# Kernel optimization log

Measured on AMD Instinct MI355X. Metric: run time of the kernel, lower is better.

## Reference

```python
import jax, jax.numpy as jnp
import numpy as np
import math

ATTN_C = 32
HEADS = 8
IN_C = 256
PAIR_C = 128
B, M, N = 1, 128, 256


def _layernorm(x, w, b, eps=1e-5):
    mu = jnp.mean(x, axis=-1, keepdims=True)
    xc = x - mu
    var = jnp.mean(xc * xc, axis=-1, keepdims=True)
    return xc * jax.lax.rsqrt(var + eps) * w + b


def setup_inputs() -> dict:
    key = jax.random.key(0)
    ks = jax.random.split(key, 10)
    s1 = 1.0 / math.sqrt(IN_C)
    s2 = 1.0 / math.sqrt(PAIR_C)
    s3 = 1.0 / math.sqrt(ATTN_C * HEADS)
    return {
        "x1d": jax.random.normal(ks[0], (B, M, N, IN_C), jnp.float32),
        "x2d": jax.random.normal(ks[1], (B, N, N, PAIR_C), jnp.float32),
        "norm_w": jnp.ones((IN_C,), jnp.float32),
        "norm_b": jnp.zeros((IN_C,), jnp.float32),
        "qkv_w": jax.random.normal(ks[2], (3 * ATTN_C * HEADS, IN_C), jnp.float32) * s1,
        "x2d_w": jax.random.normal(ks[3], (HEADS, PAIR_C), jnp.float32) * s2,
        "gate_w": jax.random.normal(ks[4], (ATTN_C * HEADS, IN_C), jnp.float32) * s1,
        "gate_b": jnp.zeros((ATTN_C * HEADS,), jnp.float32),
        "final_w": jax.random.normal(ks[5], (IN_C, ATTN_C * HEADS), jnp.float32) * s3,
        "final_b": jnp.zeros((IN_C,), jnp.float32),
    }


def reference(x1d, x2d, norm_w, norm_b, qkv_w, x2d_w, gate_w, gate_b, final_w, final_b):
    c, h = ATTN_C, HEADS
    x = _layernorm(x1d, norm_w, norm_b)                      # [B,M,N,IN_C]
    qkv = (x @ qkv_w.T).reshape(*x.shape[:-1], c, 3 * h)     # [B,M,N,c,3h]
    q, k, v = qkv[..., :h], qkv[..., h:2 * h], qkv[..., 2 * h:]
    aff = jnp.einsum('bmich,bmjch->bmijh', q, k)             # [B,M,N,N,H]
    gate = jax.nn.sigmoid(x @ gate_w.T + gate_b).reshape(*x.shape[:-1], c, h)
    factor = 1.0 / math.sqrt(c)
    bias = (x2d @ x2d_w.T) * factor                          # [B,N,N,H]
    weights = jax.nn.softmax(aff + bias[:, None], axis=-2)   # softmax over j
    out = jnp.einsum('bmrch,bmirh->bmich', v, weights) * gate
    out = out.reshape(*x.shape[:-1], c * h) @ final_w.T + final_b
    return out
```

## Files before the change

kernel.cpp:

```cpp
#include <hip/hip_runtime.h>
#include <math.h>

typedef short bf16x8 __attribute__((ext_vector_type(8)));
typedef float f32x4  __attribute__((ext_vector_type(4)));

#define NPOS 32768

#define OFF_CHI   0u
#define OFF_AHI   100663296u
#define OFF_ATTN  134217728u
#define OFF_BIAST 150994944u
#define OFF_WHI   153354240u
#define OFF_W2P   154402816u
#define OFF_GBP   154533888u

__device__ __forceinline__ short f2bf(float x) {
    unsigned int u = __float_as_uint(x);
    unsigned int r = (u + 0x7FFFu + ((u >> 16) & 1u)) >> 16;
    return (short)r;
}
__device__ __forceinline__ float bf2f(short s) {
    return __uint_as_float(((unsigned int)(unsigned short)s) << 16);
}
__device__ __forceinline__ void async_copy16(const void* g, void* l) {
    __builtin_amdgcn_global_load_lds(
        (const __attribute__((address_space(1))) unsigned int*)g,
        (__attribute__((address_space(3))) unsigned int*)l, 16, 0, 0);
}

__global__ void k_ln_cast(const float* __restrict__ x,
                          const float* __restrict__ nw, const float* __restrict__ nb,
                          short* __restrict__ Ahi) {
    int wid = (blockIdx.x * blockDim.x + threadIdx.x) >> 6;
    int lane = threadIdx.x & 63;
    const float4 v = ((const float4*)(x + (size_t)wid * 256))[lane];
    float s  = v.x + v.y + v.z + v.w;
    float ss = v.x*v.x + v.y*v.y + v.z*v.z + v.w*v.w;
    #pragma unroll
    for (int o = 32; o; o >>= 1) {
        s  += __shfl_xor(s,  o, 64);
        ss += __shfl_xor(ss, o, 64);
    }
    float mu  = s * (1.0f / 256);
    float var = ss * (1.0f / 256) - mu * mu;
    float rs  = rsqrtf(var + 1e-5f);
    const float4 wv = ((const float4*)nw)[lane];
    const float4 bv = ((const float4*)nb)[lane];
    float y[4] = {(v.x - mu) * rs * wv.x + bv.x, (v.y - mu) * rs * wv.y + bv.y,
                  (v.z - mu) * rs * wv.z + bv.z, (v.w - mu) * rs * wv.w + bv.w};
    short h4[4];
    #pragma unroll
    for (int i = 0; i < 4; ++i) h4[i] = f2bf(y[i]);
    *(short4*)(Ahi + (size_t)wid * 256 + lane * 4) = *(short4*)h4;
}

__global__ void k_castw(const float* __restrict__ qkvw, const float* __restrict__ gatew,
                        const float* __restrict__ gateb, const float* __restrict__ finalw,
                        short* __restrict__ Whi, short* __restrict__ W2p,
                        float* __restrict__ gbp) {
    int r = blockIdx.x, t = threadIdx.x;
    if (r < 1024) {
        int which = r >> 8, h = (r >> 5) & 7, c = r & 31;
        const float* src = (which < 3) ? qkvw + (size_t)(c * 24 + which * 8 + h) * 256
                                       : gatew + (size_t)(c * 8 + h) * 256;
        Whi[(size_t)r * 256 + t] = f2bf(src[t]);
    } else if (r < 1280) {
        int o = r - 1024;
        int h = t >> 5, c = t & 31;
        W2p[(size_t)o * 256 + t] = f2bf(finalw[(size_t)o * 256 + c * 8 + h]);
    } else {
        int h = t >> 5, c = t & 31;
        gbp[t] = gateb[c * 8 + h];
    }
}

__global__ __launch_bounds__(256) void k_bias2(const float* __restrict__ x2d,
                                               const float* __restrict__ x2dw,
                                               float* __restrict__ biasT) {
    __shared__ float xs[64][132];
    __shared__ float ws[8][132];
    const int t = threadIdx.x;
    const int wid0 = blockIdx.x * 64;
    #pragma unroll
    for (int r = 0; r < 8; ++r) {
        int g = r * 256 + t;
        int row = g >> 5, c4 = g & 31;
        float4 v = *(const float4*)(x2d + (size_t)(wid0 + row) * 128 + c4 * 4);
        *(float4*)&xs[row][c4 * 4] = v;
    }
    {
        int h = t >> 5, c4 = t & 31;
        *(float4*)&ws[h][c4 * 4] = *(const float4*)(x2dw + h * 128 + c4 * 4);
    }
    __syncthreads();
    const float f = 0.17677669529663687f;
    const int i = wid0 >> 8;
    #pragma unroll
    for (int kk = 0; kk < 2; ++kk) {
        int o = t + kk * 256;
        int row = o >> 3, h = o & 7;
        float acc = 0.f;
        #pragma unroll
        for (int c4 = 0; c4 < 32; ++c4) {
            float4 xv = *(const float4*)&xs[row][c4 * 4];
            float4 wv = *(const float4*)&ws[h][c4 * 4];
            acc += xv.x * wv.x + xv.y * wv.y + xv.z * wv.z + xv.w * wv.w;
        }
        int j = (wid0 & 255) + row;
        biasT[(((h * 256 + j)) << 8) + i] = acc * f;
    }
}

__global__ __launch_bounds__(256) void k_gemm1m(
    const short* __restrict__ Ahi, const short* __restrict__ Whi,
    const float* __restrict__ gbp, short* __restrict__ Chi) {
    __shared__ short As[128 * 64];
    __shared__ short Bs[128 * 64];
    const int t = threadIdx.x;
    const int wave = t >> 6, lane = t & 63, ln15 = lane & 15, quad = lane >> 4;
    const int posBase = blockIdx.x * 128;
    const int nb = blockIdx.y;
    const int i0w = (wave & 1) * 64, n0w = (wave >> 1) * 64;

    f32x4 acc[4][4];
    #pragma unroll
    for (int a = 0; a < 4; ++a)
        #pragma unroll
        for (int b = 0; b < 4; ++b) acc[a][b] = (f32x4){0.f, 0.f, 0.f, 0.f};

    for (int k0 = 0; k0 < 256; k0 += 64) {
        #pragma unroll
        for (int r = 0; r < 4; ++r) {
            int g = r * 256 + t;
            int row = g >> 3, cs = g & 7;
            int colg = cs ^ (row & 7);
            size_t aoff = (size_t)(posBase + row) * 256 + k0 + colg * 8;
            size_t boff = (size_t)(nb * 128 + row) * 256 + k0 + colg * 8;
            int ldst = (r * 256 + wave * 64) * 8;
            async_copy16(Ahi + aoff, &As[ldst]);
            async_copy16(Whi + boff, &Bs[ldst]);
        }
        __syncthreads();
        #pragma unroll
        for (int kc = 0; kc < 2; ++kc) {
            bf16x8 af[4], bfr[4];
            #pragma unroll
            for (int it = 0; it < 4; ++it) {
                int rowa = i0w + it * 16 + ln15;
                int c8a = (kc * 4 + quad) ^ (rowa & 7);
                af[it] = *(const bf16x8*)&As[rowa * 64 + c8a * 8];
                int rowb = n0w + it * 16 + ln15;
                int c8b = (kc * 4 + quad) ^ (rowb & 7);
                bfr[it] = *(const bf16x8*)&Bs[rowb * 64 + c8b * 8];
            }
            #pragma unroll
            for (int it = 0; it < 4; ++it)
                #pragma unroll
                for (int nt = 0; nt < 4; ++nt)
                    acc[it][nt] = __builtin_amdgcn_mfma_f32_16x16x32_bf16(
                        bfr[nt], af[it], acc[it][nt], 0, 0, 0);
        }
        __syncthreads();
    }
    const bool isgate = (nb >= 6);
    #pragma unroll
    for (int it = 0; it < 4; ++it) {
        size_t pos = posBase + i0w + it * 16 + ln15;
        #pragma unroll
        for (int nt = 0; nt < 4; ++nt) {
            int ncol0 = nb * 128 + n0w + nt * 16 + quad * 4;
            float v[4];
            #pragma unroll
            for (int r = 0; r < 4; ++r) v[r] = acc[it][nt][r];
            if (isgate) {
                const float4 gb = *(const float4*)&gbp[ncol0 - 768];
                v[0] = 1.0f / (1.0f + __expf(-(v[0] + gb.x)));
                v[1] = 1.0f / (1.0f + __expf(-(v[1] + gb.y)));
                v[2] = 1.0f / (1.0f + __expf(-(v[2] + gb.z)));
                v[3] = 1.0f / (1.0f + __expf(-(v[3] + gb.w)));
            }
            unsigned w0 = (unsigned)(unsigned short)f2bf(v[0])
                        | ((unsigned)(unsigned short)f2bf(v[1]) << 16);
            unsigned w1 = (unsigned)(unsigned short)f2bf(v[2])
                        | ((unsigned)(unsigned short)f2bf(v[3]) << 16);
            *(uint2*)&Chi[pos * 1024 + ncol0] = make_uint2(w0, w1);
        }
    }
}

__global__ __launch_bounds__(512) void k_attn3(
    const short* __restrict__ Chi, const float* __restrict__ biasT,
    short* __restrict__ attnB) {
    __shared__ short Khi[256 * 32];
    __shared__ short VT[32 * 264];
    __shared__ short Pl[8][16][40];

    const int mh = blockIdx.x;
    const int m = mh >> 3, h = mh & 7;
    const int t = threadIdx.x;
    const int wave = t >> 6, lane = t & 63, ln15 = lane & 15, quad = lane >> 4;
    const int i0 = wave * 32;

    #pragma unroll
    for (int r = 0; r < 2; ++r) {
        int g = r * 512 + t;
        int j = g >> 2, c16 = g & 3;
        int cs = c16 ^ (j & 3);
        const short* gp = Chi + (size_t)(m * 256 + j) * 1024 + 256 + h * 32 + cs * 8;
        async_copy16(gp, &Khi[(r * 512 + wave * 64) * 8]);
    }
    {
        int j = t & 255, c0 = (t >> 8) * 16;
        const short* vp = Chi + (size_t)(m * 256 + j) * 1024 + 512 + h * 32 + c0;
        bf16x8 v0 = *(const bf16x8*)vp;
        bf16x8 v1 = *(const bf16x8*)(vp + 8);
        #pragma unroll
        for (int c = 0; c < 8; ++c) VT[(c0 + c) * 264 + j] = v0[c];
        #pragma unroll
        for (int c = 0; c < 8; ++c) VT[(c0 + 8 + c) * 264 + j] = v1[c];
    }
    bf16x8 qhi[2];
    #pragma unroll
    for (int it = 0; it < 2; ++it) {
        int i = i0 + it * 16 + ln15;
        qhi[it] = *(const bf16x8*)(Chi + (size_t)(m * 256 + i) * 1024 + h * 32 + quad * 8);
    }
    __syncthreads();

    float lacc[2] = {0.f, 0.f};
    f32x4 Oacc[2][2];
    #pragma unroll
    for (int a = 0; a < 2; ++a) {
        Oacc[a][0] = (f32x4){0.f, 0.f, 0.f, 0.f};
        Oacc[a][1] = (f32x4){0.f, 0.f, 0.f, 0.f};
    }
    const float* bp = biasT + (size_t)h * 65536;

    for (int j0 = 0; j0 < 256; j0 += 32) {
        bf16x8 kfh[2], vf[2];
        #pragma unroll
        for (int jt = 0; jt < 2; ++jt) {
            int j = j0 + jt * 16 + ln15;
            int cs = quad ^ (j & 3);
            kfh[jt] = *(const bf16x8*)&Khi[j * 32 + cs * 8];
        }
        #pragma unroll
        for (int ct = 0; ct < 2; ++ct) {
            int c = ct * 16 + ln15;
            vf[ct] = *(const bf16x8*)&VT[c * 264 + j0 + quad * 8];
        }
        #pragma unroll
        for (int it = 0; it < 2; ++it) {
            int i = i0 + it * 16 + ln15;
            float b0[4], b1[4];
            #pragma unroll
            for (int r = 0; r < 4; ++r) {
                b0[r] = bp[(j0 + quad * 4 + r) * 256 + i];
                b1[r] = bp[(j0 + 16 + quad * 4 + r) * 256 + i];
            }
            f32x4 s0 = (f32x4){0.f, 0.f, 0.f, 0.f};
            f32x4 s1 = (f32x4){0.f, 0.f, 0.f, 0.f};
            s0 = __builtin_amdgcn_mfma_f32_16x16x32_bf16(kfh[0], qhi[it], s0, 0, 0, 0);
            s1 = __builtin_amdgcn_mfma_f32_16x16x32_bf16(kfh[1], qhi[it], s1, 0, 0, 0);
            float p[8], ps = 0.f;
            #pragma unroll
            for (int r = 0; r < 4; ++r) { p[r] = __expf(s0[r] + b0[r]); ps += p[r]; }
            #pragma unroll
            for (int r = 0; r < 4; ++r) { p[4 + r] = __expf(s1[r] + b1[r]); ps += p[4 + r]; }
            lacc[it] += ps;
            unsigned long long pw0 =
                  (unsigned long long)(unsigned short)f2bf(p[0])
                | ((unsigned long long)(unsigned short)f2bf(p[1]) << 16)
                | ((unsigned long long)(unsigned short)f2bf(p[2]) << 32)
                | ((unsigned long long)(unsigned short)f2bf(p[3]) << 48);
            unsigned long long pw1 =
                  (unsigned long long)(unsigned short)f2bf(p[4])
                | ((unsigned long long)(unsigned short)f2bf(p[5]) << 16)
                | ((unsigned long long)(unsigned short)f2bf(p[6]) << 32)
                | ((unsigned long long)(unsigned short)f2bf(p[7]) << 48);
            *(unsigned long long*)&Pl[wave][ln15][quad * 4]      = pw0;
            *(unsigned long long*)&Pl[wave][ln15][16 + quad * 4] = pw1;
            bf16x8 pf = *(const bf16x8*)&Pl[wave][ln15][quad * 8];
            Oacc[it][0] = __builtin_amdgcn_mfma_f32_16x16x32_bf16(pf, vf[0], Oacc[it][0], 0, 0, 0);
            Oacc[it][1] = __builtin_amdgcn_mfma_f32_16x16x32_bf16(pf, vf[1], Oacc[it][1], 0, 0, 0);
        }
    }
    #pragma unroll
    for (int it = 0; it < 2; ++it) {
        float l = lacc[it];
        l += __shfl_xor(l, 16, 64);
        l += __shfl_xor(l, 32, 64);
        float inv = 1.0f / l;
        float invr[4];
        #pragma unroll
        for (int r = 0; r < 4; ++r) invr[r] = __shfl(inv, quad * 4 + r, 16);
        #pragma unroll
        for (int ct = 0; ct < 2; ++ct) {
            int c = ct * 16 + ln15;
            #pragma unroll
            for (int r = 0; r < 4; ++r) {
                int i = i0 + it * 16 + quad * 4 + r;
                float g = bf2f(Chi[(size_t)(m * 256 + i) * 1024 + 768 + h * 32 + c]);
                float val = Oacc[it][ct][r] * invr[r] * g;
                attnB[(size_t)(m * 256 + i) * 256 + h * 32 + c] = f2bf(val);
            }
        }
    }
}

__global__ __launch_bounds__(256) void k_gemm2m(
    const short* __restrict__ A, const short* __restrict__ W2p,
    const float* __restrict__ fb, float* __restrict__ out) {
    __shared__ short As[128 * 64];
    __shared__ short Bs[128 * 64];
    const int t = threadIdx.x;
    const int wave = t >> 6, lane = t & 63, ln15 = lane & 15, quad = lane >> 4;
    const int posBase = blockIdx.x * 128;
    const int nb = blockIdx.y;
    const int i0w = (wave & 1) * 64, n0w = (wave >> 1) * 64;

    f32x4 acc[4][4];
    #pragma unroll
    for (int a = 0; a < 4; ++a)
        #pragma unroll
        for (int b = 0; b < 4; ++b) acc[a][b] = (f32x4){0.f, 0.f, 0.f, 0.f};

    for (int k0 = 0; k0 < 256; k0 += 64) {
        #pragma unroll
        for (int r = 0; r < 4; ++r) {
            int g = r * 256 + t;
            int row = g >> 3, cs = g & 7;
            int colg = cs ^ (row & 7);
            const short* ga = A + (size_t)(posBase + row) * 256 + k0 + colg * 8;
            async_copy16(ga, &As[(r * 256 + wave * 64) * 8]);
            const short* gb = W2p + (size_t)(nb * 128 + row) * 256 + k0 + colg * 8;
            async_copy16(gb, &Bs[(r * 256 + wave * 64) * 8]);
        }
        __syncthreads();
        #pragma unroll
        for (int kc = 0; kc < 2; ++kc) {
            bf16x8 af[4], bfr[4];
            #pragma unroll
            for (int it = 0; it < 4; ++it) {
                int rowa = i0w + it * 16 + ln15;
                int c8a = (kc * 4 + quad) ^ (rowa & 7);
                af[it] = *(const bf16x8*)&As[rowa * 64 + c8a * 8];
                int rowb = n0w + it * 16 + ln15;
                int c8b = (kc * 4 + quad) ^ (rowb & 7);
                bfr[it] = *(const bf16x8*)&Bs[rowb * 64 + c8b * 8];
            }
            #pragma unroll
            for (int it = 0; it < 4; ++it)
                #pragma unroll
                for (int nt = 0; nt < 4; ++nt)
                    acc[it][nt] = __builtin_amdgcn_mfma_f32_16x16x32_bf16(
                        bfr[nt], af[it], acc[it][nt], 0, 0, 0);
        }
        __syncthreads();
    }
    #pragma unroll
    for (int it = 0; it < 4; ++it) {
        size_t pos = posBase + i0w + it * 16 + ln15;
        #pragma unroll
        for (int nt = 0; nt < 4; ++nt) {
            int ncol0 = nb * 128 + n0w + nt * 16 + quad * 4;
            const float4 fbv = *(const float4*)&fb[ncol0];
            float4 o;
            o.x = acc[it][nt][0] + fbv.x;
            o.y = acc[it][nt][1] + fbv.y;
            o.z = acc[it][nt][2] + fbv.z;
            o.w = acc[it][nt][3] + fbv.w;
            *(float4*)&out[pos * 256 + ncol0] = o;
        }
    }
}

extern "C" void kernel_launch(void* const* d_in, const int* in_sizes, int n_in,
                              void* d_out, int out_size, void* d_ws, size_t ws_size,
                              hipStream_t stream) {
    const float* x1d     = (const float*)d_in[0];
    const float* x2d     = (const float*)d_in[1];
    const float* norm_w  = (const float*)d_in[2];
    const float* norm_b  = (const float*)d_in[3];
    const float* qkv_w   = (const float*)d_in[4];
    const float* x2d_w   = (const float*)d_in[5];
    const float* gate_w  = (const float*)d_in[6];
    const float* gate_b  = (const float*)d_in[7];
    const float* final_w = (const float*)d_in[8];
    const float* final_b = (const float*)d_in[9];
    float* out = (float*)d_out;
    char* w = (char*)d_ws;

    short* Chi   = (short*)(w + OFF_CHI);
    short* Ahi   = (short*)(w + OFF_AHI);
    short* attnB = (short*)(w + OFF_ATTN);
    float* biasT = (float*)(w + OFF_BIAST);
    short* Whi   = (short*)(w + OFF_WHI);
    short* W2p   = (short*)(w + OFF_W2P);
    float* gbp   = (float*)(w + OFF_GBP);

    k_ln_cast<<<NPOS / 4, 256, 0, stream>>>(x1d, norm_w, norm_b, Ahi);
    k_castw<<<1281, 256, 0, stream>>>(qkv_w, gate_w, gate_b, final_w, Whi, W2p, gbp);
    k_bias2<<<1024, 256, 0, stream>>>(x2d, x2d_w, biasT);
    k_gemm1m<<<dim3(256, 8), 256, 0, stream>>>(Ahi, Whi, gbp, Chi);
    k_attn3<<<1024, 512, 0, stream>>>(Chi, biasT, attnB);
    k_gemm2m<<<dim3(256, 2), 256, 0, stream>>>(attnB, W2p, final_b, out);
}
```

Baseline: 220.0 us.

## Merge preprocessing kernels into one launch and enlarge gemm1 position tile

Folds the layernorm cast, weight cast/permute and pair-bias kernels into a single block-indexed prep kernel, removing two launches and the gaps between them. The first projection GEMM now covers 256 positions per block, with each wave owning 64 rows across all 128 output columns (4x8 MFMA tiles). Each weight tile is therefore reused over more rows, at the cost of more accumulator registers and LDS and half as many blocks.

Result: slower. 227.5 us (+3.4%).

```diff
diff --git a/kernel.cpp b/kernel.cpp
--- a/kernel.cpp
+++ b/kernel.cpp
@@ -28,135 +28,141 @@
         (__attribute__((address_space(3))) unsigned int*)l, 16, 0, 0);
 }
 
-__global__ void k_ln_cast(const float* __restrict__ x,
-                          const float* __restrict__ nw, const float* __restrict__ nb,
-                          short* __restrict__ Ahi) {
-    int wid = (blockIdx.x * blockDim.x + threadIdx.x) >> 6;
-    int lane = threadIdx.x & 63;
-    const float4 v = ((const float4*)(x + (size_t)wid * 256))[lane];
-    float s  = v.x + v.y + v.z + v.w;
-    float ss = v.x*v.x + v.y*v.y + v.z*v.z + v.w*v.w;
-    #pragma unroll
-    for (int o = 32; o; o >>= 1) {
-        s  += __shfl_xor(s,  o, 64);
-        ss += __shfl_xor(ss, o, 64);
-    }
-    float mu  = s * (1.0f / 256);
-    float var = ss * (1.0f / 256) - mu * mu;
-    float rs  = rsqrtf(var + 1e-5f);
-    const float4 wv = ((const float4*)nw)[lane];
-    const float4 bv = ((const float4*)nb)[lane];
-    float y[4] = {(v.x - mu) * rs * wv.x + bv.x, (v.y - mu) * rs * wv.y + bv.y,
-                  (v.z - mu) * rs * wv.z + bv.z, (v.w - mu) * rs * wv.w + bv.w};
-    short h4[4];
-    #pragma unroll
-    for (int i = 0; i < 4; ++i) h4[i] = f2bf(y[i]);
-    *(short4*)(Ahi + (size_t)wid * 256 + lane * 4) = *(short4*)h4;
-}
-
-__global__ void k_castw(const float* __restrict__ qkvw, const float* __restrict__ gatew,
-                        const float* __restrict__ gateb, const float* __restrict__ finalw,
-                        short* __restrict__ Whi, short* __restrict__ W2p,
-                        float* __restrict__ gbp) {
-    int r = blockIdx.x, t = threadIdx.x;
-    if (r < 1024) {
-        int which = r >> 8, h = (r >> 5) & 7, c = r & 31;
-        const float* src = (which < 3) ? qkvw + (size_t)(c * 24 + which * 8 + h) * 256
-                                       : gatew + (size_t)(c * 8 + h) * 256;
-        Whi[(size_t)r * 256 + t] = f2bf(src[t]);
-    } else if (r < 1280) {
-        int o = r - 1024;
-        int h = t >> 5, c = t & 31;
-        W2p[(size_t)o * 256 + t] = f2bf(finalw[(size_t)o * 256 + c * 8 + h]);
-    } else {
-        int h = t >> 5, c = t & 31;
-        gbp[t] = gateb[c * 8 + h];
-    }
-}
-
-__global__ __launch_bounds__(256) void k_bias2(const float* __restrict__ x2d,
-                                               const float* __restrict__ x2dw,
-                                               float* __restrict__ biasT) {
+#define PREP_LN   8192
+#define PREP_CW   9473
+__global__ __launch_bounds__(256) void k_prep(
+    const float* __restrict__ x, const float* __restrict__ nw, const float* __restrict__ nb,
+    const float* __restrict__ qkvw, const float* __restrict__ gatew,
+    const float* __restrict__ gateb, const float* __restrict__ finalw,
+    const float* __restrict__ x2d, const float* __restrict__ x2dw,
+    short* __restrict__ Ahi, short* __restrict__ Whi, short* __restrict__ W2p,
+    float* __restrict__ gbp, float* __restrict__ biasT) {
     __shared__ float xs[64][132];
     __shared__ float ws[8][132];
+    const int bid = blockIdx.x;
     const int t = threadIdx.x;
-    const int wid0 = blockIdx.x * 64;
-    #pragma unroll
-    for (int r = 0; r < 8; ++r) {
-        int g = r * 256 + t;
-        int row = g >> 5, c4 = g & 31;
-        float4 v = *(const float4*)(x2d + (size_t)(wid0 + row) * 128 + c4 * 4);
-        *(float4*)&xs[row][c4 * 4] = v;
-    }
-    {
-        int h = t >> 5, c4 = t & 31;
-        *(float4*)&ws[h][c4 * 4] = *(const float4*)(x2dw + h * 128 + c4 * 4);
-    }
-    __syncthreads();
-    const float f = 0.17677669529663687f;
-    const int i = wid0 >> 8;
-    #pragma unroll
-    for (int kk = 0; kk < 2; ++kk) {
-        int o = t + kk * 256;
-        int row = o >> 3, h = o & 7;
-        float acc = 0.f;
-        #pragma unroll
-        for (int c4 = 0; c4 < 32; ++c4) {
-            float4 xv = *(const float4*)&xs[row][c4 * 4];
-            float4 wv = *(const float4*)&ws[h][c4 * 4];
-            acc += xv.x * wv.x + xv.y * wv.y + xv.z * wv.z + xv.w * wv.w;
-        }
-        int j = (wid0 & 255) + row;
-        biasT[(((h * 256 + j)) << 8) + i] = acc * f;
-    }
-}
-
-__global__ __launch_bounds__(256) void k_gemm1m(
+
+    if (bid < PREP_LN) {
+        int wid = (bid * 256 + t) >> 6;
+        int lane = t & 63;
+        const float4 v = ((const float4*)(x + (size_t)wid * 256))[lane];
+        float s  = v.x + v.y + v.z + v.w;
+        float ss = v.x*v.x + v.y*v.y + v.z*v.z + v.w*v.w;
+        #pragma unroll
+        for (int o = 32; o; o >>= 1) {
+            s  += __shfl_xor(s,  o, 64);
+            ss += __shfl_xor(ss, o, 64);
+        }
+        float mu  = s * (1.0f / 256);
+        float var = ss * (1.0f / 256) - mu * mu;
+        float rs  = rsqrtf(var + 1e-5f);
+        const float4 wv = ((const float4*)nw)[lane];
+        const float4 bv = ((const float4*)nb)[lane];
+        float y[4] = {(v.x - mu) * rs * wv.x + bv.x, (v.y - mu) * rs * wv.y + bv.y,
+                      (v.z - mu) * rs * wv.z + bv.z, (v.w - mu) * rs * wv.w + bv.w};
+        short h4[4];
+        #pragma unroll
+        for (int i = 0; i < 4; ++i) h4[i] = f2bf(y[i]);
+        *(short4*)(Ahi + (size_t)wid * 256 + lane * 4) = *(short4*)h4;
+    } else if (bid < PREP_CW) {
+        int r = bid - PREP_LN;
+        if (r < 1024) {
+            int which = r >> 8, h = (r >> 5) & 7, c = r & 31;
+            const float* src = (which < 3) ? qkvw + (size_t)(c * 24 + which * 8 + h) * 256
+                                           : gatew + (size_t)(c * 8 + h) * 256;
+            Whi[(size_t)r * 256 + t] = f2bf(src[t]);
+        } else if (r < 1280) {
+            int o = r - 1024;
+            int h = t >> 5, c = t & 31;
+            W2p[(size_t)o * 256 + t] = f2bf(finalw[(size_t)o * 256 + c * 8 + h]);
+        } else {
+            int h = t >> 5, c = t & 31;
+            gbp[t] = gateb[c * 8 + h];
+        }
+    } else {
+        const int wid0 = (bid - PREP_CW) * 64;
+        #pragma unroll
+        for (int r = 0; r < 8; ++r) {
+            int g = r * 256 + t;
+            int row = g >> 5, c4 = g & 31;
+            float4 v = *(const float4*)(x2d + (size_t)(wid0 + row) * 128 + c4 * 4);
+            *(float4*)&xs[row][c4 * 4] = v;
+        }
+        {
+            int h = t >> 5, c4 = t & 31;
+            *(float4*)&ws[h][c4 * 4] = *(const float4*)(x2dw + h * 128 + c4 * 4);
+        }
+        __syncthreads();
+        const float f = 0.17677669529663687f;
+        const int i = wid0 >> 8;
+        #pragma unroll
+        for (int kk = 0; kk < 2; ++kk) {
+            int o = t + kk * 256;
+            int row = o >> 3, h = o & 7;
+            float acc = 0.f;
+            #pragma unroll
+            for (int c4 = 0; c4 < 32; ++c4) {
+                float4 xv = *(const float4*)&xs[row][c4 * 4];
+                float4 wv = *(const float4*)&ws[h][c4 * 4];
+                acc += xv.x * wv.x + xv.y * wv.y + xv.z * wv.z + xv.w * wv.w;
+            }
+            int j = (wid0 & 255) + row;
+            biasT[(((h * 256 + j)) << 8) + i] = acc * f;
+        }
+    }
+}
+
+__global__ __launch_bounds__(256, 2) void k_gemm1m(
     const short* __restrict__ Ahi, const short* __restrict__ Whi,
     const float* __restrict__ gbp, short* __restrict__ Chi) {
-    __shared__ short As[128 * 64];
+    __shared__ short As[256 * 64];
     __shared__ short Bs[128 * 64];
     const int t = threadIdx.x;
     const int wave = t >> 6, lane = t & 63, ln15 = lane & 15, quad = lane >> 4;
-    const int posBase = blockIdx.x * 128;
+    const int posBase = blockIdx.x * 256;
     const int nb = blockIdx.y;
-    const int i0w = (wave & 1) * 64, n0w = (wave >> 1) * 64;
-
-    f32x4 acc[4][4];
+
+    f32x4 acc[4][8];
     #pragma unroll
     for (int a = 0; a < 4; ++a)
         #pragma unroll
-        for (int b = 0; b < 4; ++b) acc[a][b] = (f32x4){0.f, 0.f, 0.f, 0.f};
+        for (int b = 0; b < 8; ++b) acc[a][b] = (f32x4){0.f, 0.f, 0.f, 0.f};
 
     for (int k0 = 0; k0 < 256; k0 += 64) {
+        #pragma unroll
+        for (int r = 0; r < 8; ++r) {
+            int g = r * 256 + t;
+            int row = g >> 3, cs = g & 7;
+            int colg = cs ^ (row & 7);
+            async_copy16(Ahi + (size_t)(posBase + row) * 256 + k0 + colg * 8, &As[g * 8]);
+        }
         #pragma unroll
         for (int r = 0; r < 4; ++r) {
             int g = r * 256 + t;
             int row = g >> 3, cs = g & 7;
             int colg = cs ^ (row & 7);
-            size_t aoff = (size_t)(posBase + row) * 256 + k0 + colg * 8;
-            size_t boff = (size_t)(nb * 128 + row) * 256 + k0 + colg * 8;
-            int ldst = (r * 256 + wave * 64) * 8;
-            async_copy16(Ahi + aoff, &As[ldst]);
-            async_copy16(Whi + boff, &Bs[ldst]);
+            async_copy16(Whi + (size_t)(nb * 128 + row) * 256 + k0 + colg * 8, &Bs[g * 8]);
         }
         __syncthreads();
         #pragma unroll
         for (int kc = 0; kc < 2; ++kc) {
-            bf16x8 af[4], bfr[4];
+            bf16x8 af[4], bfr[8];
             #pragma unroll
             for (int it = 0; it < 4; ++it) {
-                int rowa = i0w + it * 16 + ln15;
+                int rowa = wave * 64 + it * 16 + ln15;
                 int c8a = (kc * 4 + quad) ^ (rowa & 7);
                 af[it] = *(const bf16x8*)&As[rowa * 64 + c8a * 8];
-                int rowb = n0w + it * 16 + ln15;
+            }
+            #pragma unroll
+            for (int nt = 0; nt < 8; ++nt) {
+                int rowb = nt * 16 + ln15;
                 int c8b = (kc * 4 + quad) ^ (rowb & 7);
-                bfr[it] = *(const bf16x8*)&Bs[rowb * 64 + c8b * 8];
+                bfr[nt] = *(const bf16x8*)&Bs[rowb * 64 + c8b * 8];
             }
             #pragma unroll
             for (int it = 0; it < 4; ++it)
                 #pragma unroll
-                for (int nt = 0; nt < 4; ++nt)
+                for (int nt = 0; nt < 8; ++nt)
                     acc[it][nt] = __builtin_amdgcn_mfma_f32_16x16x32_bf16(
                         bfr[nt], af[it], acc[it][nt], 0, 0, 0);
         }
@@ -165,10 +171,10 @@
     const bool isgate = (nb >= 6);
     #pragma unroll
     for (int it = 0; it < 4; ++it) {
-        size_t pos = posBase + i0w + it * 16 + ln15;
-        #pragma unroll
-        for (int nt = 0; nt < 4; ++nt) {
-            int ncol0 = nb * 128 + n0w + nt * 16 + quad * 4;
+        size_t pos = posBase + wave * 64 + it * 16 + ln15;
+        #pragma unroll
+        for (int nt = 0; nt < 8; ++nt) {
+            int ncol0 = nb * 128 + nt * 16 + quad * 4;
             float v[4];
             #pragma unroll
             for (int r = 0; r < 4; ++r) v[r] = acc[it][nt][r];
@@ -399,10 +405,9 @@
     short* W2p   = (short*)(w + OFF_W2P);
     float* gbp   = (float*)(w + OFF_GBP);
 
-    k_ln_cast<<<NPOS / 4, 256, 0, stream>>>(x1d, norm_w, norm_b, Ahi);
-    k_castw<<<1281, 256, 0, stream>>>(qkv_w, gate_w, gate_b, final_w, Whi, W2p, gbp);
-    k_bias2<<<1024, 256, 0, stream>>>(x2d, x2d_w, biasT);
-    k_gemm1m<<<dim3(256, 8), 256, 0, stream>>>(Ahi, Whi, gbp, Chi);
+    k_prep<<<10497, 256, 0, stream>>>(x1d, norm_w, norm_b, qkv_w, gate_w, gate_b,
+                                      final_w, x2d, x2d_w, Ahi, Whi, W2p, gbp, biasT);
+    k_gemm1m<<<dim3(128, 8), 256, 0, stream>>>(Ahi, Whi, gbp, Chi);
     k_attn3<<<1024, 512, 0, stream>>>(Chi, biasT, attnB);
     k_gemm2m<<<dim3(256, 2), 256, 0, stream>>>(attnB, W2p, final_b, out);
 }
```
